# Kernel tuning notes

Measured on AMD Instinct MI355X. Metric: run time of the kernel, lower is better.

Reference implementation:

```python
import jax, jax.numpy as jnp
import numpy as np

EMBED = 1024
HEADS = 16
HEAD_DIM = EMBED // HEADS
N, S = 2, 2048


def setup_inputs() -> dict:
    key = jax.random.key(0)
    ks = jax.random.split(key, 8)
    scale_p = 1.0 / np.sqrt(HEAD_DIM)
    return {
        "queries": jax.random.normal(ks[0], (N, S, EMBED), jnp.float32),
        "keys": jax.random.normal(ks[1], (N, S, EMBED), jnp.float32),
        "values": jax.random.normal(ks[2], (N, S, EMBED), jnp.float32),
        # per-head projection weights, torch Linear convention: y = x @ W.T
        "Wq": jax.random.normal(ks[3], (HEAD_DIM, HEAD_DIM), jnp.float32) * scale_p,
        "Wk": jax.random.normal(ks[4], (HEAD_DIM, HEAD_DIM), jnp.float32) * scale_p,
        "Wv": jax.random.normal(ks[5], (HEAD_DIM, HEAD_DIM), jnp.float32) * scale_p,
        "Wo": jax.random.normal(ks[6], (EMBED, EMBED), jnp.float32) * (1.0 / np.sqrt(EMBED)),
        "bo": jax.random.normal(ks[7], (EMBED,), jnp.float32) * 0.01,
    }


def reference(queries, keys, values, Wq, Wk, Wv, Wo, bo):
    n, sq, e = queries.shape
    sk = keys.shape[1]
    # split heads: (N, S, H, D)
    q = queries.reshape(n, sq, HEADS, HEAD_DIM)
    k = keys.reshape(n, sk, HEADS, HEAD_DIM)
    v = values.reshape(n, sk, HEADS, HEAD_DIM)
    # per-head linear projections (weights shared across heads), torch Linear: x @ W.T
    q = jnp.einsum('nshd,ed->nshe', q, Wq)
    k = jnp.einsum('nshd,ed->nshe', k, Wk)
    v = jnp.einsum('nshd,ed->nshe', v, Wv)
    # attention scores (N, H, Q, K); NOTE: scaled by sqrt(embed_size), as in source
    energy = jnp.einsum('nqhd,nkhd->nhqk', q, k)
    attention = jax.nn.softmax(energy / jnp.sqrt(jnp.float32(EMBED)), axis=3)
    out = jnp.einsum('nhql,nlhd->nqhd', attention, v).reshape(n, sq, EMBED)
    return out @ Wo.T + bo
```

## Files before the change

kernel.cpp:

```cpp
#include <hip/hip_runtime.h>
#include <hip/hip_bf16.h>

#define NB 2
#define SS 2048
#define EE 1024
#define HH 16
#define DD 64
#define NHD (NB*HH)
#define KT 64

#define QSCALE 0.04508422002777998f

typedef _Float16 half8 __attribute__((ext_vector_type(8)));
typedef _Float16 half4 __attribute__((ext_vector_type(4)));
typedef float floatx4 __attribute__((ext_vector_type(4)));

__device__ __forceinline__ half8 cvt8(const float* p) {
    float4 x = *(const float4*)p;
    float4 y = *(const float4*)(p + 4);
    half8 h = { (_Float16)x.x, (_Float16)x.y, (_Float16)x.z, (_Float16)x.w,
                (_Float16)y.x, (_Float16)y.y, (_Float16)y.z, (_Float16)y.w };
    return h;
}

__global__ __launch_bounds__(256) void proj_kernel(
    const float* __restrict__ Q, const float* __restrict__ K, const float* __restrict__ V,
    const float* __restrict__ Wq, const float* __restrict__ Wk, const float* __restrict__ Wv,
    _Float16* __restrict__ Qp, _Float16* __restrict__ Kp, _Float16* __restrict__ Vt)
{
    int t = threadIdx.x, lane = t & 63, wid = t >> 6;
    int lr = lane & 15, lg = lane >> 4;
    int g0 = blockIdx.x * 64 + wid * 16;

    size_t obase[4];
    int    svals[4];
    int    dbase_nh[4];
    #pragma unroll
    for (int r = 0; r < 4; ++r) {
        int g = g0 + lg * 4 + r;
        int h = g & 15, s = (g >> 4) & (SS - 1), n = g >> 15;
        int nh = n * HH + h;
        obase[r] = ((size_t)nh * SS + s) * DD;
        svals[r] = s;
        dbase_nh[r] = nh;
    }

    const float* tens[3] = {Q, K, V};
    const float* wts[3]  = {Wq, Wk, Wv};

    #pragma unroll
    for (int x = 0; x < 3; ++x) {
        const float* Xr = tens[x] + (size_t)(g0 + lr) * DD + lg * 8;
        half8 a0 = cvt8(Xr);
        half8 a1 = cvt8(Xr + 32);
        floatx4 acc[4];
        #pragma unroll
        for (int ns = 0; ns < 4; ++ns) {
            const float* Wr = wts[x] + (size_t)(ns * 16 + lr) * DD + lg * 8;
            half8 b0 = cvt8(Wr);
            half8 b1 = cvt8(Wr + 32);
            floatx4 c = (floatx4){0.f, 0.f, 0.f, 0.f};
            c = __builtin_amdgcn_mfma_f32_16x16x32_f16(a0, b0, c, 0, 0, 0);
            c = __builtin_amdgcn_mfma_f32_16x16x32_f16(a1, b1, c, 0, 0, 0);
            acc[ns] = c;
        }
        if (x == 0) {
            #pragma unroll
            for (int ns = 0; ns < 4; ++ns)
                #pragma unroll
                for (int r = 0; r < 4; ++r)
                    Qp[obase[r] + ns * 16 + lr] = (_Float16)(acc[ns][r] * QSCALE);
        } else if (x == 1) {
            #pragma unroll
            for (int ns = 0; ns < 4; ++ns)
                #pragma unroll
                for (int r = 0; r < 4; ++r)
                    Kp[obase[r] + ns * 16 + lr] = (_Float16)acc[ns][r];
        } else {
            #pragma unroll
            for (int ns = 0; ns < 4; ++ns)
                #pragma unroll
                for (int r = 0; r < 4; ++r)
                    Vt[((size_t)dbase_nh[r] * DD + ns * 16 + lr) * SS + svals[r]]
                        = (_Float16)acc[ns][r];
        }
    }
}

__global__ __launch_bounds__(256) void attn_kernel(
    const _Float16* __restrict__ Qp, const _Float16* __restrict__ Kp,
    const _Float16* __restrict__ Vt, _Float16* __restrict__ Of)
{
    int b = blockIdx.x;
    int slot = b >> 3;
    int nh = (b & 7) * 4 + (slot & 3);
    int qt = slot >> 2;
    int n = nh >> 4, h = nh & 15;
    int t = threadIdx.x;
    int lane = t & 63, wid = t >> 6;
    int lr = lane & 15;
    int lg = lane >> 4;

    __shared__ __align__(16) _Float16 kbuf[2][KT][DD + 8];
    __shared__ __align__(16) _Float16 vbuf[2][DD][KT + 8];
    __shared__ __align__(16) _Float16 plds[4][16][KT + 8];

    const _Float16* Qb = Qp + ((size_t)nh * SS + qt * 64 + wid * 16) * DD;
    const _Float16* Kb = Kp + (size_t)nh * SS * DD;
    const _Float16* Vb = Vt + (size_t)nh * DD * SS;

    half8 qf0 = *(const half8*)(Qb + (size_t)lr * DD + lg * 8);
    half8 qf1 = *(const half8*)(Qb + (size_t)lr * DD + 32 + lg * 8);

    int sr = t >> 3, sc = (t & 7) * 8;

    {
        half8 k0 = *(const half8*)(Kb + (size_t)sr * DD + sc);
        half8 k1 = *(const half8*)(Kb + (size_t)(sr + 32) * DD + sc);
        half8 v0 = *(const half8*)(Vb + (size_t)sr * SS + sc);
        half8 v1 = *(const half8*)(Vb + (size_t)(sr + 32) * SS + sc);
        *(half8*)(&kbuf[0][sr][sc]) = k0;
        *(half8*)(&kbuf[0][sr + 32][sc]) = k1;
        *(half8*)(&vbuf[0][sr][sc]) = v0;
        *(half8*)(&vbuf[0][sr + 32][sc]) = v1;
    }
    __syncthreads();

    floatx4 oacc[4];
    #pragma unroll
    for (int ns = 0; ns < 4; ++ns) oacc[ns] = (floatx4){0.f, 0.f, 0.f, 0.f};
    float lsumF = 0.f;

    int p = 0;
    for (int kb = 0; kb < SS; kb += KT, p ^= 1) {
        int kn = (kb + KT) & (SS - 1);
        half8 sk0 = *(const half8*)(Kb + (size_t)(kn + sr) * DD + sc);
        half8 sk1 = *(const half8*)(Kb + (size_t)(kn + sr + 32) * DD + sc);
        half8 sv0 = *(const half8*)(Vb + (size_t)sr * SS + kn + sc);
        half8 sv1 = *(const half8*)(Vb + (size_t)(sr + 32) * SS + kn + sc);

        half8 kf[4][2];
        #pragma unroll
        for (int ns = 0; ns < 4; ++ns) {
            const _Float16* kr = &kbuf[p][ns * 16 + lr][lg * 8];
            kf[ns][0] = *(const half8*)(kr);
            kf[ns][1] = *(const half8*)(kr + 32);
        }
        floatx4 sc_[4];
        #pragma unroll
        for (int ns = 0; ns < 4; ++ns) {
            floatx4 c = (floatx4){0.f, 0.f, 0.f, 0.f};
            c = __builtin_amdgcn_mfma_f32_16x16x32_f16(kf[ns][0], qf0, c, 0, 0, 0);
            c = __builtin_amdgcn_mfma_f32_16x16x32_f16(kf[ns][1], qf1, c, 0, 0, 0);
            sc_[ns] = c;
        }
        half8 vf[4][2];
        #pragma unroll
        for (int ns = 0; ns < 4; ++ns) {
            const _Float16* vr = &vbuf[p][ns * 16 + lr][lg * 8];
            vf[ns][0] = *(const half8*)(vr);
            vf[ns][1] = *(const half8*)(vr + 32);
        }
        #pragma unroll
        for (int ns = 0; ns < 4; ++ns) {
            float p0 = exp2f(fminf(sc_[ns][0], 50.f));
            float p1 = exp2f(fminf(sc_[ns][1], 50.f));
            float p2 = exp2f(fminf(sc_[ns][2], 50.f));
            float p3 = exp2f(fminf(sc_[ns][3], 50.f));
            lsumF += (p0 + p1) + (p2 + p3);
            half4 v = { (_Float16)p0, (_Float16)p1, (_Float16)p2, (_Float16)p3 };
            *(half4*)(&plds[wid][lr][ns * 16 + lg * 4]) = v;
        }
        asm volatile("s_waitcnt lgkmcnt(0)" ::: "memory");
        half8 pf0 = *(const half8*)(&plds[wid][lr][lg * 8]);
        half8 pf1 = *(const half8*)(&plds[wid][lr][32 + lg * 8]);
        #pragma unroll
        for (int ns = 0; ns < 4; ++ns) {
            oacc[ns] = __builtin_amdgcn_mfma_f32_16x16x32_f16(pf0, vf[ns][0], oacc[ns], 0, 0, 0);
            oacc[ns] = __builtin_amdgcn_mfma_f32_16x16x32_f16(pf1, vf[ns][1], oacc[ns], 0, 0, 0);
        }
        *(half8*)(&kbuf[p ^ 1][sr][sc]) = sk0;
        *(half8*)(&kbuf[p ^ 1][sr + 32][sc]) = sk1;
        *(half8*)(&vbuf[p ^ 1][sr][sc]) = sv0;
        *(half8*)(&vbuf[p ^ 1][sr + 32][sc]) = sv1;
        __syncthreads();
    }

    float s = lsumF;
    s += __shfl_xor(s, 16, 64);
    s += __shfl_xor(s, 32, 64);
    float linv[4];
    #pragma unroll
    for (int r = 0; r < 4; ++r)
        linv[r] = 1.f / __shfl(s, lg * 4 + r, 64);

    _Float16* Ob = Of + ((size_t)n * SS + qt * 64 + wid * 16) * EE + h * DD;
    #pragma unroll
    for (int ns = 0; ns < 4; ++ns)
        #pragma unroll
        for (int r = 0; r < 4; ++r)
            Ob[(size_t)(lg * 4 + r) * EE + ns * 16 + lr] = (_Float16)(oacc[ns][r] * linv[r]);
}

__global__ __launch_bounds__(256) void wconv_kernel(
    const float* __restrict__ W, _Float16* __restrict__ Wf)
{
    int i = (blockIdx.x * 256 + threadIdx.x) * 8;
    *(half8*)(Wf + i) = cvt8(W + i);
}

__global__ __launch_bounds__(256, 1) void oproj_kernel(
    const _Float16* __restrict__ Of, const _Float16* __restrict__ Wf,
    const float* __restrict__ bo, float* __restrict__ out)
{
    int b = blockIdx.x;
    int nb = b & 7, mb = b >> 3;
    int t = threadIdx.x, lane = t & 63, wid = t >> 6;
    int wm = wid >> 1, wn = wid & 1;
    int lr = lane & 15, lg = lane >> 4;
    int m0 = mb * 128, n0 = nb * 128;

    __shared__ __align__(16) _Float16 As[2][128][72];
    __shared__ __align__(16) _Float16 Bs[2][128][72];

    int srow = t >> 1, scol = (t & 1) * 32;
    const _Float16* Ag = Of + (size_t)(m0 + srow) * EE + scol;
    const _Float16* Bg = Wf + (size_t)(n0 + srow) * EE + scol;

    floatx4 acc[4][4];
    #pragma unroll
    for (int sm = 0; sm < 4; ++sm)
        #pragma unroll
        for (int sn = 0; sn < 4; ++sn) acc[sm][sn] = (floatx4){0.f, 0.f, 0.f, 0.f};

    #pragma unroll
    for (int j = 0; j < 4; ++j) {
        *(half8*)(&As[0][srow][scol + j * 8]) = *(const half8*)(Ag + j * 8);
        *(half8*)(&Bs[0][srow][scol + j * 8]) = *(const half8*)(Bg + j * 8);
    }
    __syncthreads();

    int p = 0;
    for (int kb = 0; kb < EE; kb += 64, p ^= 1) {
        int kn = kb + 64;
        half8 sa[4], sb[4];
        if (kn < EE) {
            #pragma unroll
            for (int j = 0; j < 4; ++j) {
                sa[j] = *(const half8*)(Ag + kn + j * 8);
                sb[j] = *(const half8*)(Bg + kn + j * 8);
            }
        }
        #pragma unroll
        for (int kk = 0; kk < 2; ++kk) {
            half8 af[4], bf[4];
            #pragma unroll
            for (int s = 0; s < 4; ++s) {
                af[s] = *(const half8*)(&As[p][wm * 64 + s * 16 + lr][kk * 32 + lg * 8]);
                bf[s] = *(const half8*)(&Bs[p][wn * 64 + s * 16 + lr][kk * 32 + lg * 8]);
            }
            #pragma unroll
            for (int sm = 0; sm < 4; ++sm)
                #pragma unroll
                for (int sn = 0; sn < 4; ++sn)
                    acc[sm][sn] = __builtin_amdgcn_mfma_f32_16x16x32_f16(
                        af[sm], bf[sn], acc[sm][sn], 0, 0, 0);
        }
        if (kn < EE) {
            #pragma unroll
            for (int j = 0; j < 4; ++j) {
                *(half8*)(&As[p ^ 1][srow][scol + j * 8]) = sa[j];
                *(half8*)(&Bs[p ^ 1][srow][scol + j * 8]) = sb[j];
            }
        }
        __syncthreads();
    }

    #pragma unroll
    for (int sn = 0; sn < 4; ++sn) {
        int nn = n0 + wn * 64 + sn * 16 + lr;
        float bn = bo[nn];
        #pragma unroll
        for (int sm = 0; sm < 4; ++sm) {
            #pragma unroll
            for (int r = 0; r < 4; ++r)
                out[(size_t)(m0 + wm * 64 + sm * 16 + lg * 4 + r) * EE + nn]
                    = acc[sm][sn][r] + bn;
        }
    }
}

extern "C" void kernel_launch(void* const* d_in, const int* in_sizes, int n_in,
                              void* d_out, int out_size, void* d_ws, size_t ws_size,
                              hipStream_t stream)
{
    const float* Q  = (const float*)d_in[0];
    const float* K  = (const float*)d_in[1];
    const float* V  = (const float*)d_in[2];
    const float* Wq = (const float*)d_in[3];
    const float* Wk = (const float*)d_in[4];
    const float* Wv = (const float*)d_in[5];
    const float* Wo = (const float*)d_in[6];
    const float* bo = (const float*)d_in[7];
    float* out = (float*)d_out;

    const size_t NSE = (size_t)NB * SS * EE;
    _Float16* Qp = (_Float16*)d_ws;
    _Float16* Kp = Qp + NSE;
    _Float16* Vt = Kp + NSE;
    _Float16* Of = Vt + NSE;
    _Float16* Wf = Of + NSE;

    proj_kernel<<<1024, 256, 0, stream>>>(Q, K, V, Wq, Wk, Wv, Qp, Kp, Vt);
    wconv_kernel<<<(EE * EE) / (256 * 8), 256, 0, stream>>>(Wo, Wf);
    attn_kernel<<<NHD * (SS / 64), 256, 0, stream>>>(Qp, Kp, Vt, Of);
    oproj_kernel<<<256, 256, 0, stream>>>(Of, Wf, bo, out);
}
```

Measured before the change: 240.9 us.

## Swizzle attention LDS tiles and stage V transpose through shared memory

The attention kernel's K, V and P shared-memory tiles drop row padding and use an XOR-swizzled 64-column layout to avoid bank conflicts, which shrinks LDS use. Launch bounds now request 4 blocks per multiprocessor. The projection kernel is reorganised per (batch-head, sequence-tile). Its V output is written to shared memory first and then stored to the transposed Vt with contiguous vector writes, replacing scattered 2-byte strided stores. This adds a block barrier in the projection kernel and index arithmetic for the swizzle.

```diff
diff --git a/kernel.cpp b/kernel.cpp
--- a/kernel.cpp
+++ b/kernel.cpp
@@ -23,6 +23,10 @@
     return h;
 }
 
+__device__ __forceinline__ int swz64(int row, int colh) {
+    return (row << 6) + ((((colh >> 3) ^ (row & 7)) << 3) | (colh & 7));
+}
+
 __global__ __launch_bounds__(256) void proj_kernel(
     const float* __restrict__ Q, const float* __restrict__ K, const float* __restrict__ V,
     const float* __restrict__ Wq, const float* __restrict__ Wk, const float* __restrict__ Wv,
@@ -30,27 +34,22 @@
 {
     int t = threadIdx.x, lane = t & 63, wid = t >> 6;
     int lr = lane & 15, lg = lane >> 4;
-    int g0 = blockIdx.x * 64 + wid * 16;
-
-    size_t obase[4];
-    int    svals[4];
-    int    dbase_nh[4];
-    #pragma unroll
-    for (int r = 0; r < 4; ++r) {
-        int g = g0 + lg * 4 + r;
-        int h = g & 15, s = (g >> 4) & (SS - 1), n = g >> 15;
-        int nh = n * HH + h;
-        obase[r] = ((size_t)nh * SS + s) * DD;
-        svals[r] = s;
-        dbase_nh[r] = nh;
-    }
+    int b = blockIdx.x;
+    int nh = b >> 5, st = b & 31;
+    int n = nh >> 4, h = nh & 15;
+
+    __shared__ __align__(16) _Float16 vt[DD][72];
+
+    const size_t xoff = ((size_t)n * SS + st * 64 + wid * 16 + lr) * EE
+                        + (size_t)h * DD + lg * 8;
+    const size_t qob = ((size_t)nh * SS + st * 64 + wid * 16 + lg * 4) * DD;
 
     const float* tens[3] = {Q, K, V};
     const float* wts[3]  = {Wq, Wk, Wv};
 
     #pragma unroll
     for (int x = 0; x < 3; ++x) {
-        const float* Xr = tens[x] + (size_t)(g0 + lr) * DD + lg * 8;
+        const float* Xr = tens[x] + xoff;
         half8 a0 = cvt8(Xr);
         half8 a1 = cvt8(Xr + 32);
         floatx4 acc[4];
@@ -69,25 +68,31 @@
             for (int ns = 0; ns < 4; ++ns)
                 #pragma unroll
                 for (int r = 0; r < 4; ++r)
-                    Qp[obase[r] + ns * 16 + lr] = (_Float16)(acc[ns][r] * QSCALE);
+                    Qp[qob + (size_t)r * DD + ns * 16 + lr] = (_Float16)(acc[ns][r] * QSCALE);
         } else if (x == 1) {
             #pragma unroll
             for (int ns = 0; ns < 4; ++ns)
                 #pragma unroll
                 for (int r = 0; r < 4; ++r)
-                    Kp[obase[r] + ns * 16 + lr] = (_Float16)acc[ns][r];
+                    Kp[qob + (size_t)r * DD + ns * 16 + lr] = (_Float16)acc[ns][r];
         } else {
             #pragma unroll
             for (int ns = 0; ns < 4; ++ns)
                 #pragma unroll
                 for (int r = 0; r < 4; ++r)
-                    Vt[((size_t)dbase_nh[r] * DD + ns * 16 + lr) * SS + svals[r]]
-                        = (_Float16)acc[ns][r];
-        }
-    }
-}
-
-__global__ __launch_bounds__(256) void attn_kernel(
+                    vt[ns * 16 + lr][wid * 16 + lg * 4 + r] = (_Float16)acc[ns][r];
+        }
+    }
+    __syncthreads();
+    {
+        int d = t >> 2, q4 = (t & 3) * 16;
+        _Float16* dst = Vt + ((size_t)nh * DD + d) * SS + st * 64 + q4;
+        *(half8*)dst       = *(const half8*)(&vt[d][q4]);
+        *(half8*)(dst + 8) = *(const half8*)(&vt[d][q4 + 8]);
+    }
+}
+
+__global__ __launch_bounds__(256, 4) void attn_kernel(
     const _Float16* __restrict__ Qp, const _Float16* __restrict__ Kp,
     const _Float16* __restrict__ Vt, _Float16* __restrict__ Of)
 {
@@ -101,9 +106,9 @@
     int lr = lane & 15;
     int lg = lane >> 4;
 
-    __shared__ __align__(16) _Float16 kbuf[2][KT][DD + 8];
-    __shared__ __align__(16) _Float16 vbuf[2][DD][KT + 8];
-    __shared__ __align__(16) _Float16 plds[4][16][KT + 8];
+    __shared__ __align__(16) _Float16 kbuf[2][KT * DD];
+    __shared__ __align__(16) _Float16 vbuf[2][DD * KT];
+    __shared__ __align__(16) _Float16 plds[4][16 * 64];
 
     const _Float16* Qb = Qp + ((size_t)nh * SS + qt * 64 + wid * 16) * DD;
     const _Float16* Kb = Kp + (size_t)nh * SS * DD;
@@ -119,10 +124,10 @@
         half8 k1 = *(const half8*)(Kb + (size_t)(sr + 32) * DD + sc);
         half8 v0 = *(const half8*)(Vb + (size_t)sr * SS + sc);
         half8 v1 = *(const half8*)(Vb + (size_t)(sr + 32) * SS + sc);
-        *(half8*)(&kbuf[0][sr][sc]) = k0;
-        *(half8*)(&kbuf[0][sr + 32][sc]) = k1;
-        *(half8*)(&vbuf[0][sr][sc]) = v0;
-        *(half8*)(&vbuf[0][sr + 32][sc]) = v1;
+        *(half8*)(&kbuf[0][swz64(sr, sc)]) = k0;
+        *(half8*)(&kbuf[0][swz64(sr + 32, sc)]) = k1;
+        *(half8*)(&vbuf[0][swz64(sr, sc)]) = v0;
+        *(half8*)(&vbuf[0][swz64(sr + 32, sc)]) = v1;
     }
     __syncthreads();
 
@@ -142,9 +147,8 @@
         half8 kf[4][2];
         #pragma unroll
         for (int ns = 0; ns < 4; ++ns) {
-            const _Float16* kr = &kbuf[p][ns * 16 + lr][lg * 8];
-            kf[ns][0] = *(const half8*)(kr);
-            kf[ns][1] = *(const half8*)(kr + 32);
+            kf[ns][0] = *(const half8*)(&kbuf[p][swz64(ns * 16 + lr, lg * 8)]);
+            kf[ns][1] = *(const half8*)(&kbuf[p][swz64(ns * 16 + lr, 32 + lg * 8)]);
         }
         floatx4 sc_[4];
         #pragma unroll
@@ -157,9 +161,8 @@
         half8 vf[4][2];
         #pragma unroll
         for (int ns = 0; ns < 4; ++ns) {
-            const _Float16* vr = &vbuf[p][ns * 16 + lr][lg * 8];
-            vf[ns][0] = *(const half8*)(vr);
-            vf[ns][1] = *(const half8*)(vr + 32);
+            vf[ns][0] = *(const half8*)(&vbuf[p][swz64(ns * 16 + lr, lg * 8)]);
+            vf[ns][1] = *(const half8*)(&vbuf[p][swz64(ns * 16 + lr, 32 + lg * 8)]);
         }
         #pragma unroll
         for (int ns = 0; ns < 4; ++ns) {
@@ -169,20 +172,20 @@
             float p3 = exp2f(fminf(sc_[ns][3], 50.f));
             lsumF += (p0 + p1) + (p2 + p3);
             half4 v = { (_Float16)p0, (_Float16)p1, (_Float16)p2, (_Float16)p3 };
-            *(half4*)(&plds[wid][lr][ns * 16 + lg * 4]) = v;
+            *(half4*)(&plds[wid][swz64(lr, ns * 16 + lg * 4)]) = v;
         }
         asm volatile("s_waitcnt lgkmcnt(0)" ::: "memory");
-        half8 pf0 = *(const half8*)(&plds[wid][lr][lg * 8]);
-        half8 pf1 = *(const half8*)(&plds[wid][lr][32 + lg * 8]);
+        half8 pf0 = *(const half8*)(&plds[wid][swz64(lr, lg * 8)]);
+        half8 pf1 = *(const half8*)(&plds[wid][swz64(lr, 32 + lg * 8)]);
         #pragma unroll
         for (int ns = 0; ns < 4; ++ns) {
             oacc[ns] = __builtin_amdgcn_mfma_f32_16x16x32_f16(pf0, vf[ns][0], oacc[ns], 0, 0, 0);
             oacc[ns] = __builtin_amdgcn_mfma_f32_16x16x32_f16(pf1, vf[ns][1], oacc[ns], 0, 0, 0);
         }
-        *(half8*)(&kbuf[p ^ 1][sr][sc]) = sk0;
-        *(half8*)(&kbuf[p ^ 1][sr + 32][sc]) = sk1;
-        *(half8*)(&vbuf[p ^ 1][sr][sc]) = sv0;
-        *(half8*)(&vbuf[p ^ 1][sr + 32][sc]) = sv1;
+        *(half8*)(&kbuf[p ^ 1][swz64(sr, sc)]) = sk0;
+        *(half8*)(&kbuf[p ^ 1][swz64(sr + 32, sc)]) = sk1;
+        *(half8*)(&vbuf[p ^ 1][swz64(sr, sc)]) = sv0;
+        *(half8*)(&vbuf[p ^ 1][swz64(sr + 32, sc)]) = sv1;
         __syncthreads();
     }
 
```

After: 211.8 us. 12.1% less time.
